# Performance work log

Hardware: AMD Instinct MI355X
Metric: run time of the kernel (lower is better)

## Reference

```python
import jax, jax.numpy as jnp
import numpy as np

N_EMBED = 1024
N_HEADS = 16


def setup_inputs() -> dict:
    key = jax.random.key(0)
    k_x, k_wa, k_wp = jax.random.split(key, 3)
    B, T, C = 2, 2048, N_EMBED
    x = jax.random.normal(k_x, (B, T, C), dtype=jnp.float32)
    # flax Dense default: lecun_normal kernel, zero bias; use scaled normal here
    w_attn = jax.random.normal(k_wa, (C, 3 * C), dtype=jnp.float32) / np.sqrt(C)
    b_attn = jnp.zeros((3 * C,), dtype=jnp.float32)
    w_proj = jax.random.normal(k_wp, (C, C), dtype=jnp.float32) / np.sqrt(C)
    b_proj = jnp.zeros((C,), dtype=jnp.float32)
    return {"x": x, "w_attn": w_attn, "b_attn": b_attn,
            "w_proj": w_proj, "b_proj": b_proj}


def reference(x, w_attn, b_attn, w_proj, b_proj):
    B, T, C = x.shape
    H = N_HEADS
    D = C // H
    qkv = x @ w_attn + b_attn                      # [B,T,3C]
    q, k, v = jnp.split(qkv, 3, axis=-1)           # each [B,T,C]
    q = q.reshape(B, T, H, D).swapaxes(1, 2)       # [B,H,T,D]
    k = k.reshape(B, T, H, D).swapaxes(1, 2)
    v = v.reshape(B, T, H, D).swapaxes(1, 2)
    att = jnp.einsum('bhid,bhjd->bhij', q, k) * (1.0 / jnp.sqrt(D))
    causal = jnp.tril(jnp.ones((T, T), dtype=bool))
    att = jnp.where(causal, att, -jnp.inf)
    att = jax.nn.softmax(att, axis=-1)
    y = jnp.einsum('bhij,bhjd->bhid', att, v)      # [B,H,T,D]
    y = y.swapaxes(1, 2).reshape(B, T, C)
    return y @ w_proj + b_proj
```

## Files before the change

### kernel.cpp

```cpp
#include <hip/hip_runtime.h>
#include <hip/hip_bf16.h>

typedef __bf16 bf16x8 __attribute__((ext_vector_type(8)));
typedef float f32x4 __attribute__((ext_vector_type(4)));
typedef float f32x16 __attribute__((ext_vector_type(16)));
typedef unsigned short u16;
typedef unsigned int u32;
typedef u16 u16x8 __attribute__((ext_vector_type(8)));
typedef u32 u32x4 __attribute__((ext_vector_type(4)));

#define SM_SCALE 0.1803368801111244f

__device__ inline u16 tobf(float f) {
  u32 u = __builtin_bit_cast(u32, f);
  u32 r = (u + 0x7fffu + ((u >> 16) & 1u)) >> 16;
  return (u16)r;
}

__device__ inline float frombf(u16 h) {
  return __builtin_bit_cast(float, (u32)h << 16);
}

__device__ inline void gload_lds16(const void* g, void* lds) {
  __builtin_amdgcn_global_load_lds(
      (const __attribute__((address_space(1))) u32*)g,
      (__attribute__((address_space(3))) u32*)lds, 16, 0, 0);
}

__global__ void convert_f32_bf16(const float* __restrict__ in,
                                 u16* __restrict__ out, int n8) {
  int i = blockIdx.x * blockDim.x + threadIdx.x;
  int stride = gridDim.x * blockDim.x;
  for (; i < n8; i += stride) {
    const float4* p = (const float4*)in + (size_t)i * 2;
    float4 a = p[0], b = p[1];
    u16x8 v;
    v[0] = tobf(a.x); v[1] = tobf(a.y); v[2] = tobf(a.z); v[3] = tobf(a.w);
    v[4] = tobf(b.x); v[5] = tobf(b.y); v[6] = tobf(b.z); v[7] = tobf(b.w);
    *(u16x8*)(out + (size_t)i * 8) = v;
  }
}

__global__ void transpose_w(const float* __restrict__ in,
                            u16* __restrict__ out, int K, int N) {
  __shared__ float tile[32][33];
  int nbx = N >> 5;
  int bx = blockIdx.x % nbx, by = blockIdx.x / nbx;
  int k0 = by << 5, n0 = bx << 5;
  int tx = threadIdx.x & 31, ty = threadIdx.x >> 5;
#pragma unroll
  for (int j = 0; j < 4; ++j) {
    int row = ty + j * 8;
    tile[row][tx] = in[(size_t)(k0 + row) * N + n0 + tx];
  }
  __syncthreads();
#pragma unroll
  for (int j = 0; j < 4; ++j) {
    int row = ty + j * 8;
    out[(size_t)(n0 + row) * K + k0 + tx] = tobf(tile[tx][row]);
  }
}

template <int EPI, int BN>
__global__ __launch_bounds__(256) void gemm_bt(
    const u16* __restrict__ A, const u16* __restrict__ Bt,
    const float* __restrict__ bias,
    u16* __restrict__ o0, u16* __restrict__ o1, u16* __restrict__ o2,
    float* __restrict__ fo, int M, int N, int K) {
  constexpr int NF = BN / 32;
  __shared__ __align__(16) u16 As[2][128 * 64];
  __shared__ __align__(16) u16 Bs[2][BN * 64];
  const int tid = threadIdx.x;
  const int lane = tid & 63;
  const int wave = tid >> 6;
  const int nbn = N / BN;
  int bid = (int)blockIdx.x;
  const int cpx = (int)gridDim.x >> 3;
  bid = (bid & 7) * cpx + (bid >> 3);
  const int bm = bid / nbn, bn = bid % nbn;
  const int m0 = bm << 7, n0 = bn * BN;
  const int wr = wave >> 1, wc = wave & 1;
  const int r15 = lane & 15, g = lane >> 4;

  f32x4 acc[4][NF] = {};

#define GSTAGE(buf, kt)                                                    \
  do {                                                                     \
    _Pragma("unroll")                                                      \
    for (int j = 0; j < 4; ++j) {                                          \
      int c = j * 4 + wave;                                                \
      int byte0 = c * 1024 + lane * 16;                                    \
      int row = byte0 >> 7;                                                \
      int colb = (byte0 & 127) ^ ((row & 7) << 4);                         \
      gload_lds16(A + (size_t)(m0 + row) * K + (kt) * 64 + (colb >> 1),    \
                  (char*)As[(buf)] + c * 1024);                            \
    }                                                                      \
    _Pragma("unroll")                                                      \
    for (int j = 0; j < NF; ++j) {                                         \
      int c = j * 4 + wave;                                                \
      int byte0 = c * 1024 + lane * 16;                                    \
      int row = byte0 >> 7;                                                \
      int colb = (byte0 & 127) ^ ((row & 7) << 4);                         \
      gload_lds16(Bt + (size_t)(n0 + row) * K + (kt) * 64 + (colb >> 1),   \
                  (char*)Bs[(buf)] + c * 1024);                            \
    }                                                                      \
  } while (0)

  const int nkt = K >> 6;
  GSTAGE(0, 0);
  asm volatile("s_waitcnt vmcnt(0)");
  __syncthreads();
  for (int kt = 0; kt < nkt; ++kt) {
    const int cur = kt & 1;
    if (kt + 1 < nkt) GSTAGE(cur ^ 1, kt + 1);
#pragma unroll
    for (int kk = 0; kk < 2; ++kk) {
      bf16x8 af[4], bf[NF];
#pragma unroll
      for (int i = 0; i < 4; ++i) {
        int rowA = wr * 64 + i * 16 + r15;
        int ca = (kk * 64 + 16 * g) ^ ((rowA & 7) << 4);
        af[i] = *(const bf16x8*)((const char*)As[cur] + rowA * 128 + ca);
      }
#pragma unroll
      for (int j2 = 0; j2 < NF; ++j2) {
        int rowB = wc * (BN / 2) + j2 * 16 + r15;
        int cb = (kk * 64 + 16 * g) ^ ((rowB & 7) << 4);
        bf[j2] = *(const bf16x8*)((const char*)Bs[cur] + rowB * 128 + cb);
      }
#pragma unroll
      for (int i = 0; i < 4; ++i)
#pragma unroll
        for (int j2 = 0; j2 < NF; ++j2)
          acc[i][j2] = __builtin_amdgcn_mfma_f32_16x16x32_bf16(
              af[i], bf[j2], acc[i][j2], 0, 0, 0);
    }
    asm volatile("s_waitcnt vmcnt(0)");
    __syncthreads();
  }
#undef GSTAGE

#pragma unroll
  for (int j2 = 0; j2 < NF; ++j2) {
    const int n = n0 + wc * (BN / 2) + j2 * 16 + r15;
    const float bv = bias[n];
#pragma unroll
    for (int i = 0; i < 4; ++i) {
      const int mb = m0 + wr * 64 + i * 16 + g * 4;
      float v[4];
#pragma unroll
      for (int rr = 0; rr < 4; ++rr) v[rr] = acc[i][j2][rr] + bv;
      if (EPI == 1) {
#pragma unroll
        for (int rr = 0; rr < 4; ++rr) fo[(size_t)(mb + rr) * N + n] = v[rr];
      } else {
        const int b = mb >> 11, t = mb & 2047;
        const int sec = n >> 10, nn = n & 1023;
        const int h = nn >> 6, d = nn & 63;
        const int bh = b * 16 + h;
        if (sec == 0) {
          u16* base = o0 + ((size_t)bh * 2048 + t) * 64 + d;
#pragma unroll
          for (int rr = 0; rr < 4; ++rr) base[rr * 64] = tobf(v[rr] * SM_SCALE);
        } else if (sec == 1) {
          u16* kb = o1 +
                    (((size_t)(bh * 32 + (t >> 6)) * 4 + (d >> 4)) * 2) * 512 +
                    ((d >> 3) & 1) * 256 + (d & 7);
          const int tb = t & 63;
#pragma unroll
          for (int rr = 0; rr < 4; ++rr) {
            int r = tb + rr;
            kb[(r >> 5) * 512 + (r & 31) * 8] = tobf(v[rr]);
          }
        } else {
          const int tl = t & 63;
          u16* vb = o2 +
                    ((((size_t)(bh * 32 + (t >> 6)) * 4 + (tl >> 4)) * 2 +
                      (d >> 5)) * 512) +
                    ((tl >> 3) & 1) * 256 + (d & 31) * 8 + (tl & 7);
          u32* p = (u32*)vb;
          p[0] = (u32)tobf(v[0]) | ((u32)tobf(v[1]) << 16);
          p[1] = (u32)tobf(v[2]) | ((u32)tobf(v[3]) << 16);
        }
      }
    }
  }
}

static __device__ const signed char PT_C[34] =
    {15,15,15,15,14,14,14,13,13,13,12,12,12,11,11,11,10,10,10,9,9,8,8,7,7,6,6,5,5,4,3,2,1,0};
static __device__ const signed char PT_K0[34] =
    {0,8,16,24,0,10,20,0,9,18,0,8,17,0,8,16,0,7,14,0,10,0,9,0,8,0,7,0,6,0,0,0,0,0};
static __device__ const signed char PT_KN[34] =
    {8,16,24,32,10,20,30,9,18,28,8,17,26,8,16,24,7,14,22,10,20,9,18,8,16,7,14,6,12,10,8,6,4,2};
static __device__ const signed char PT_SL[34] =
    {-1,0,1,2,-1,3,4,-1,5,6,-1,7,8,-1,9,10,-1,11,12,-1,13,-1,14,-1,15,-1,16,-1,17,-2,-2,-2,-2,-2};

__global__ __launch_bounds__(256) void attn_kernel(
    const u16* __restrict__ qb, const u16* __restrict__ kpk,
    const u16* __restrict__ vpk, u16* __restrict__ yb,
    u16* __restrict__ party, float* __restrict__ partM) {
  const int tid = threadIdx.x;
  const int lane = tid & 63;
  const int w = tid >> 6;
  const int q31 = lane & 31, hi = lane >> 5;
  const int bx = blockIdx.x;
  const int pid = bx >> 5, bh = bx & 31;
  const int c = PT_C[pid];
  const int kt0 = PT_K0[pid], ktN = PT_KN[pid];
  const int slot = PT_SL[pid];

  const int q0 = c * 128 + w * 32;
  const int qg = q0 + q31;
  const int qmax = q0 + 31;
  const int ktEnd = min(ktN, (qmax >> 6) + 1);

  const u16* qrow = qb + ((size_t)bh * 2048 + qg) * 64;
  bf16x8 aq[4];
#pragma unroll
  for (int ks = 0; ks < 4; ++ks)
    aq[ks] = *(const bf16x8*)(qrow + ks * 16 + 8 * hi);

  f32x16 o0 = {}, o1 = {};
  float m = -INFINITY, l = 0.f;

  const u16* kbh = kpk + (size_t)bh * 32 * 4096 + lane * 8;
  const u16* vbh = vpk + (size_t)bh * 32 * 4096 + lane * 8;

  for (int kt = kt0; kt < ktEnd; ++kt) {
    const u16* kp = kbh + (size_t)kt * 4096;
    const u16* vp = vbh + (size_t)kt * 4096;

    bf16x8 kf[8];
#pragma unroll
    for (int j = 0; j < 8; ++j) kf[j] = *(const bf16x8*)(kp + j * 512);

    f32x16 s0 = {}, s1 = {};
    __builtin_amdgcn_s_setprio(1);
#pragma unroll
    for (int ks = 0; ks < 4; ++ks) {
      s0 = __builtin_amdgcn_mfma_f32_32x32x16_bf16(kf[2 * ks], aq[ks], s0, 0, 0, 0);
      s1 = __builtin_amdgcn_mfma_f32_32x32x16_bf16(kf[2 * ks + 1], aq[ks], s1, 0, 0, 0);
    }
    __builtin_amdgcn_s_setprio(0);

    if (kt * 64 + 63 > q0) {
      const int thr = qg - kt * 64;
#pragma unroll
      for (int r = 0; r < 16; ++r) {
        const int off = (r & 3) + 8 * (r >> 2) + 4 * hi;
        if (off > thr) s0[r] = -INFINITY;
        if (off + 32 > thr) s1[r] = -INFINITY;
      }
    }
    f32x16 mx;
#pragma unroll
    for (int r = 0; r < 16; ++r) mx[r] = fmaxf(s0[r], s1[r]);
#pragma unroll
    for (int st = 8; st >= 1; st >>= 1)
#pragma unroll
      for (int r = 0; r < st; ++r) mx[r] = fmaxf(mx[r], mx[r + st]);
    float mt = fmaxf(mx[0], __shfl_xor(mx[0], 32, 64));

    if (kt == kt0) {
      m = mt;
    } else if (__any(mt > m + 8.f)) {
      float mnew = fmaxf(m, mt);
      float alpha = exp2f(m - mnew);
      m = mnew;
      l *= alpha;
#pragma unroll
      for (int r = 0; r < 16; ++r) {
        o0[r] *= alpha;
        o1[r] *= alpha;
      }
    }
#pragma unroll
    for (int r = 0; r < 16; ++r) {
      s0[r] = exp2f(s0[r] - m);
      s1[r] = exp2f(s1[r] - m);
    }
    {
      float la = 0.f, lb = 0.f, lc2 = 0.f, ld = 0.f;
#pragma unroll
      for (int r = 0; r < 16; r += 2) {
        la += s0[r];
        lb += s0[r + 1];
        lc2 += s1[r];
        ld += s1[r + 1];
      }
      l += (la + lb) + (lc2 + ld);
    }
    u32 W[16];
#pragma unroll
    for (int i2 = 0; i2 < 8; ++i2) {
      asm("v_cvt_pk_bf16_f32 %0, %1, %2"
          : "=v"(W[i2]) : "v"(s0[2 * i2]), "v"(s0[2 * i2 + 1]));
      asm("v_cvt_pk_bf16_f32 %0, %1, %2"
          : "=v"(W[8 + i2]) : "v"(s1[2 * i2]), "v"(s1[2 * i2 + 1]));
    }
#pragma unroll
    for (int b4 = 0; b4 < 16; b4 += 4) {
      asm("v_permlane32_swap_b32 %0, %1" : "+v"(W[b4]), "+v"(W[b4 + 2]));
      asm("v_permlane32_swap_b32 %0, %1" : "+v"(W[b4 + 1]), "+v"(W[b4 + 3]));
    }
    bf16x8 vf[8];
#pragma unroll
    for (int j = 0; j < 8; ++j) vf[j] = *(const bf16x8*)(vp + j * 512);

    __builtin_amdgcn_s_setprio(1);
#pragma unroll
    for (int ks = 0; ks < 4; ++ks) {
      u32x4 pwv = {W[4 * ks], W[4 * ks + 1], W[4 * ks + 2], W[4 * ks + 3]};
      bf16x8 pf = __builtin_bit_cast(bf16x8, pwv);
      o0 = __builtin_amdgcn_mfma_f32_32x32x16_bf16(vf[2 * ks], pf, o0, 0, 0, 0);
      o1 = __builtin_amdgcn_mfma_f32_32x32x16_bf16(vf[2 * ks + 1], pf, o1, 0, 0, 0);
    }
    __builtin_amdgcn_s_setprio(0);
  }

  l += __shfl_xor(l, 32, 64);
  float inv = 1.0f / l;

  u32* dst;
  if (slot >= 0) {
    dst = (u32*)(party +
                 ((size_t)((slot * 32 + bh) * 128 + w * 32 + q31)) * 64);
  } else {
    int b = bh >> 4, hd = bh & 15;
    dst = (u32*)(yb + ((size_t)b * 2048 + qg) * 1024 + hd * 64);
  }
#pragma unroll
  for (int r = 0; r < 16; r += 2) {
    int d = (r & 3) + 8 * (r >> 2) + 4 * hi;
    dst[d >> 1] = (u32)tobf(o0[r] * inv) | ((u32)tobf(o0[r + 1] * inv) << 16);
    dst[(d + 32) >> 1] =
        (u32)tobf(o1[r] * inv) | ((u32)tobf(o1[r + 1] * inv) << 16);
  }
  if (slot != -2 && hi == 0)
    partM[(pid * 32 + bh) * 128 + w * 32 + q31] = m + log2f(l);
}

static __device__ const signed char CB_PID[11] = {0,4,7,10,13,16,19,21,23,25,27};
static __device__ const signed char CB_P[11]   = {4,3,3,3,3,3,2,2,2,2,2};
static __device__ const signed char CB_SL[11]  = {0,3,5,7,9,11,13,14,15,16,17};

__global__ __launch_bounds__(256) void attn_combine(
    const u16* __restrict__ party, const float* __restrict__ partM,
    u16* __restrict__ yb) {
  const int gi = blockIdx.x;
  const int ci = gi >> 5, bh = gi & 31;
  const int c = 15 - ci;
  const int pidb = CB_PID[ci], P = CB_P[ci], slb = CB_SL[ci];
  const int row = threadIdx.x >> 1, off = (threadIdx.x & 1) * 32;

  const float M0 = partM[((pidb + 0) * 32 + bh) * 128 + row];
  const float M1 = partM[((pidb + 1) * 32 + bh) * 128 + row];
  const float M2 = (P > 2) ? partM[((pidb + 2) * 32 + bh) * 128 + row] : -INFINITY;
  const float M3 = (P > 3) ? partM[((pidb + 3) * 32 + bh) * 128 + row] : -INFINITY;
  const float Mm = fmaxf(fmaxf(M0, M1), fmaxf(M2, M3));
  const float w0 = exp2f(M0 - Mm), w1 = exp2f(M1 - Mm);
  const float w2 = exp2f(M2 - Mm), w3 = exp2f(M3 - Mm);
  const float inv = 1.f / (w0 + w1 + w2 + w3);

  const int b = bh >> 4, head = bh & 15, t = c * 128 + row;
  u16* y = yb + ((size_t)b * 2048 + t) * 1024 + head * 64 + off;

  float acc[32];
#pragma unroll
  for (int j = 0; j < 4; ++j) {
    u16x8 a = *(const u16x8*)(y + j * 8);
#pragma unroll
    for (int e = 0; e < 8; ++e) acc[j * 8 + e] = frombf(a[e]) * w0;
  }
  {
    const u16* p1 = party + ((size_t)((slb + 0) * 32 + bh) * 128 + row) * 64 + off;
#pragma unroll
    for (int j = 0; j < 4; ++j) {
      u16x8 a = *(const u16x8*)(p1 + j * 8);
#pragma unroll
      for (int e = 0; e < 8; ++e) acc[j * 8 + e] += frombf(a[e]) * w1;
    }
  }
  if (P > 2) {
    const u16* p2 = party + ((size_t)((slb + 1) * 32 + bh) * 128 + row) * 64 + off;
#pragma unroll
    for (int j = 0; j < 4; ++j) {
      u16x8 a = *(const u16x8*)(p2 + j * 8);
#pragma unroll
      for (int e = 0; e < 8; ++e) acc[j * 8 + e] += frombf(a[e]) * w2;
    }
  }
  if (P > 3) {
    const u16* p3 = party + ((size_t)((slb + 2) * 32 + bh) * 128 + row) * 64 + off;
#pragma unroll
    for (int j = 0; j < 4; ++j) {
      u16x8 a = *(const u16x8*)(p3 + j * 8);
#pragma unroll
      for (int e = 0; e < 8; ++e) acc[j * 8 + e] += frombf(a[e]) * w3;
    }
  }
#pragma unroll
  for (int j = 0; j < 4; ++j) {
    u16x8 ov;
#pragma unroll
    for (int e = 0; e < 8; ++e) ov[e] = tobf(acc[j * 8 + e] * inv);
    *(u16x8*)(y + j * 8) = ov;
  }
}

extern "C" void kernel_launch(void* const* d_in, const int* in_sizes, int n_in,
                              void* d_out, int out_size, void* d_ws,
                              size_t ws_size, hipStream_t stream) {
  const float* x = (const float*)d_in[0];
  const float* w_attn = (const float*)d_in[1];
  const float* b_attn = (const float*)d_in[2];
  const float* w_proj = (const float*)d_in[3];
  const float* b_proj = (const float*)d_in[4];
  float* out = (float*)d_out;
  char* ws = (char*)d_ws;

  u16* xb = (u16*)ws;
  u16* wat = (u16*)(ws + (8ull << 20));
  u16* wpt = (u16*)(ws + (14ull << 20));
  u16* qbuf = (u16*)(ws + (16ull << 20));
  u16* kpk = (u16*)(ws + (24ull << 20));
  u16* vpk = (u16*)(ws + (32ull << 20));
  u16* yb = (u16*)(ws + (40ull << 20));
  u16* party = (u16*)ws;
  float* partM = (float*)(ws + (10ull << 20));

  convert_f32_bf16<<<2048, 256, 0, stream>>>(x, xb, (4096 * 1024) / 8);
  transpose_w<<<3072, 256, 0, stream>>>(w_attn, wat, 1024, 3072);
  transpose_w<<<1024, 256, 0, stream>>>(w_proj, wpt, 1024, 1024);
  gemm_bt<0, 192><<<32 * 16, 256, 0, stream>>>(xb, wat, b_attn, qbuf, kpk,
                                               vpk, nullptr, 4096, 3072, 1024);
  attn_kernel<<<34 * 32, 256, 0, stream>>>(qbuf, kpk, vpk, yb, party, partM);
  attn_combine<<<352, 256, 0, stream>>>(party, partM, yb);
  gemm_bt<1, 64><<<32 * 16, 256, 0, stream>>>(yb, wpt, b_proj, nullptr,
                                              nullptr, nullptr, out, 4096,
                                              1024, 1024);
}
```

Measured before the change: 118.1 us.

## Merge prep kernels into one launch and double-buffer K loads in attention

Combines the x-to-bf16 conversion and the two weight transposes into a single prep kernel, removing two kernel launches and their gaps. In the attention loop, the next tile's K fragments are now prefetched into an alternating register buffer, and the V loads are issued right after the QK MFMAs, so global-load latency overlaps the softmax work. This raises register pressure through the extra K buffer, which could lower occupancy or cause spills.

```diff
diff --git a/kernel.cpp b/kernel.cpp
--- a/kernel.cpp
+++ b/kernel.cpp
@@ -27,27 +27,14 @@
       (__attribute__((address_space(3))) u32*)lds, 16, 0, 0);
 }
 
-__global__ void convert_f32_bf16(const float* __restrict__ in,
-                                 u16* __restrict__ out, int n8) {
-  int i = blockIdx.x * blockDim.x + threadIdx.x;
-  int stride = gridDim.x * blockDim.x;
-  for (; i < n8; i += stride) {
-    const float4* p = (const float4*)in + (size_t)i * 2;
-    float4 a = p[0], b = p[1];
-    u16x8 v;
-    v[0] = tobf(a.x); v[1] = tobf(a.y); v[2] = tobf(a.z); v[3] = tobf(a.w);
-    v[4] = tobf(b.x); v[5] = tobf(b.y); v[6] = tobf(b.z); v[7] = tobf(b.w);
-    *(u16x8*)(out + (size_t)i * 8) = v;
-  }
-}
-
-__global__ void transpose_w(const float* __restrict__ in,
-                            u16* __restrict__ out, int K, int N) {
+__device__ __forceinline__ void transpose_body(const float* __restrict__ in,
+                                               u16* __restrict__ out, int K,
+                                               int N, int bxg, int tid) {
   __shared__ float tile[32][33];
   int nbx = N >> 5;
-  int bx = blockIdx.x % nbx, by = blockIdx.x / nbx;
+  int bx = bxg % nbx, by = bxg / nbx;
   int k0 = by << 5, n0 = bx << 5;
-  int tx = threadIdx.x & 31, ty = threadIdx.x >> 5;
+  int tx = tid & 31, ty = tid >> 5;
 #pragma unroll
   for (int j = 0; j < 4; ++j) {
     int row = ty + j * 8;
@@ -58,6 +45,26 @@
   for (int j = 0; j < 4; ++j) {
     int row = ty + j * 8;
     out[(size_t)(n0 + row) * K + k0 + tx] = tobf(tile[tx][row]);
+  }
+}
+
+__global__ __launch_bounds__(256) void prep_kernel(
+    const float* __restrict__ x, u16* __restrict__ xb,
+    const float* __restrict__ wa, u16* __restrict__ wat,
+    const float* __restrict__ wp, u16* __restrict__ wpt) {
+  const int b = blockIdx.x, tid = threadIdx.x;
+  if (b < 2048) {
+    int i = b * 256 + tid;
+    const float4* p = (const float4*)x + (size_t)i * 2;
+    float4 a = p[0], c = p[1];
+    u16x8 v;
+    v[0] = tobf(a.x); v[1] = tobf(a.y); v[2] = tobf(a.z); v[3] = tobf(a.w);
+    v[4] = tobf(c.x); v[5] = tobf(c.y); v[6] = tobf(c.z); v[7] = tobf(c.w);
+    *(u16x8*)(xb + (size_t)i * 8) = v;
+  } else if (b < 5120) {
+    transpose_body(wa, wat, 1024, 3072, b - 2048, tid);
+  } else {
+    transpose_body(wp, wpt, 1024, 1024, b - 5120, tid);
   }
 }
 
@@ -196,6 +203,100 @@
 static __device__ const signed char PT_SL[34] =
     {-1,0,1,2,-1,3,4,-1,5,6,-1,7,8,-1,9,10,-1,11,12,-1,13,-1,14,-1,15,-1,16,-1,17,-2,-2,-2,-2,-2};
 
+__device__ __forceinline__ void attn_tile(
+    int kt, int kt0, int ktEnd, int q0, int qg, int hi,
+    const u16* __restrict__ kbh, const u16* __restrict__ vbh,
+    const bf16x8 (&aq)[4], const bf16x8 (&KF)[8], bf16x8 (&KN)[8],
+    bf16x8 (&vf)[8], f32x16& o0, f32x16& o1, float& m, float& l) {
+  f32x16 s0 = {}, s1 = {};
+  __builtin_amdgcn_s_setprio(1);
+#pragma unroll
+  for (int ks = 0; ks < 4; ++ks) {
+    s0 = __builtin_amdgcn_mfma_f32_32x32x16_bf16(KF[2 * ks], aq[ks], s0, 0, 0, 0);
+    s1 = __builtin_amdgcn_mfma_f32_32x32x16_bf16(KF[2 * ks + 1], aq[ks], s1, 0, 0, 0);
+  }
+  __builtin_amdgcn_s_setprio(0);
+
+  const u16* vp = vbh + (size_t)kt * 4096;
+#pragma unroll
+  for (int j = 0; j < 8; ++j) vf[j] = *(const bf16x8*)(vp + j * 512);
+  if (kt + 1 < ktEnd) {
+    const u16* kp2 = kbh + (size_t)(kt + 1) * 4096;
+#pragma unroll
+    for (int j = 0; j < 8; ++j) KN[j] = *(const bf16x8*)(kp2 + j * 512);
+  }
+
+  if (kt * 64 + 63 > q0) {
+    const int thr = qg - kt * 64;
+#pragma unroll
+    for (int r = 0; r < 16; ++r) {
+      const int off = (r & 3) + 8 * (r >> 2) + 4 * hi;
+      if (off > thr) s0[r] = -INFINITY;
+      if (off + 32 > thr) s1[r] = -INFINITY;
+    }
+  }
+  f32x16 mx;
+#pragma unroll
+  for (int r = 0; r < 16; ++r) mx[r] = fmaxf(s0[r], s1[r]);
+#pragma unroll
+  for (int st = 8; st >= 1; st >>= 1)
+#pragma unroll
+    for (int r = 0; r < st; ++r) mx[r] = fmaxf(mx[r], mx[r + st]);
+  float mt = fmaxf(mx[0], __shfl_xor(mx[0], 32, 64));
+
+  if (kt == kt0) {
+    m = mt;
+  } else if (__any(mt > m + 8.f)) {
+    float mnew = fmaxf(m, mt);
+    float alpha = exp2f(m - mnew);
+    m = mnew;
+    l *= alpha;
+#pragma unroll
+    for (int r = 0; r < 16; ++r) {
+      o0[r] *= alpha;
+      o1[r] *= alpha;
+    }
+  }
+#pragma unroll
+  for (int r = 0; r < 16; ++r) {
+    s0[r] = exp2f(s0[r] - m);
+    s1[r] = exp2f(s1[r] - m);
+  }
+  {
+    float la = 0.f, lb = 0.f, lc2 = 0.f, ld = 0.f;
+#pragma unroll
+    for (int r = 0; r < 16; r += 2) {
+      la += s0[r];
+      lb += s0[r + 1];
+      lc2 += s1[r];
+      ld += s1[r + 1];
+    }
+    l += (la + lb) + (lc2 + ld);
+  }
+  u32 W[16];
+#pragma unroll
+  for (int i2 = 0; i2 < 8; ++i2) {
+    asm("v_cvt_pk_bf16_f32 %0, %1, %2"
+        : "=v"(W[i2]) : "v"(s0[2 * i2]), "v"(s0[2 * i2 + 1]));
+    asm("v_cvt_pk_bf16_f32 %0, %1, %2"
+        : "=v"(W[8 + i2]) : "v"(s1[2 * i2]), "v"(s1[2 * i2 + 1]));
+  }
+#pragma unroll
+  for (int b4 = 0; b4 < 16; b4 += 4) {
+    asm("v_permlane32_swap_b32 %0, %1" : "+v"(W[b4]), "+v"(W[b4 + 2]));
+    asm("v_permlane32_swap_b32 %0, %1" : "+v"(W[b4 + 1]), "+v"(W[b4 + 3]));
+  }
+  __builtin_amdgcn_s_setprio(1);
+#pragma unroll
+  for (int ks = 0; ks < 4; ++ks) {
+    u32x4 pwv = {W[4 * ks], W[4 * ks + 1], W[4 * ks + 2], W[4 * ks + 3]};
+    bf16x8 pf = __builtin_bit_cast(bf16x8, pwv);
+    o0 = __builtin_amdgcn_mfma_f32_32x32x16_bf16(vf[2 * ks], pf, o0, 0, 0, 0);
+    o1 = __builtin_amdgcn_mfma_f32_32x32x16_bf16(vf[2 * ks + 1], pf, o1, 0, 0, 0);
+  }
+  __builtin_amdgcn_s_setprio(0);
+}
+
 __global__ __launch_bounds__(256) void attn_kernel(
     const u16* __restrict__ qb, const u16* __restrict__ kpk,
     const u16* __restrict__ vpk, u16* __restrict__ yb,
@@ -227,96 +328,19 @@
   const u16* kbh = kpk + (size_t)bh * 32 * 4096 + lane * 8;
   const u16* vbh = vpk + (size_t)bh * 32 * 4096 + lane * 8;
 
-  for (int kt = kt0; kt < ktEnd; ++kt) {
-    const u16* kp = kbh + (size_t)kt * 4096;
-    const u16* vp = vbh + (size_t)kt * 4096;
-
-    bf16x8 kf[8];
-#pragma unroll
-    for (int j = 0; j < 8; ++j) kf[j] = *(const bf16x8*)(kp + j * 512);
-
-    f32x16 s0 = {}, s1 = {};
-    __builtin_amdgcn_s_setprio(1);
-#pragma unroll
-    for (int ks = 0; ks < 4; ++ks) {
-      s0 = __builtin_amdgcn_mfma_f32_32x32x16_bf16(kf[2 * ks], aq[ks], s0, 0, 0, 0);
-      s1 = __builtin_amdgcn_mfma_f32_32x32x16_bf16(kf[2 * ks + 1], aq[ks], s1, 0, 0, 0);
-    }
-    __builtin_amdgcn_s_setprio(0);
-
-    if (kt * 64 + 63 > q0) {
-      const int thr = qg - kt * 64;
-#pragma unroll
-      for (int r = 0; r < 16; ++r) {
-        const int off = (r & 3) + 8 * (r >> 2) + 4 * hi;
-        if (off > thr) s0[r] = -INFINITY;
-        if (off + 32 > thr) s1[r] = -INFINITY;
-      }
-    }
-    f32x16 mx;
-#pragma unroll
-    for (int r = 0; r < 16; ++r) mx[r] = fmaxf(s0[r], s1[r]);
-#pragma unroll
-    for (int st = 8; st >= 1; st >>= 1)
-#pragma unroll
-      for (int r = 0; r < st; ++r) mx[r] = fmaxf(mx[r], mx[r + st]);
-    float mt = fmaxf(mx[0], __shfl_xor(mx[0], 32, 64));
-
-    if (kt == kt0) {
-      m = mt;
-    } else if (__any(mt > m + 8.f)) {
-      float mnew = fmaxf(m, mt);
-      float alpha = exp2f(m - mnew);
-      m = mnew;
-      l *= alpha;
-#pragma unroll
-      for (int r = 0; r < 16; ++r) {
-        o0[r] *= alpha;
-        o1[r] *= alpha;
-      }
-    }
-#pragma unroll
-    for (int r = 0; r < 16; ++r) {
-      s0[r] = exp2f(s0[r] - m);
-      s1[r] = exp2f(s1[r] - m);
-    }
-    {
-      float la = 0.f, lb = 0.f, lc2 = 0.f, ld = 0.f;
-#pragma unroll
-      for (int r = 0; r < 16; r += 2) {
-        la += s0[r];
-        lb += s0[r + 1];
-        lc2 += s1[r];
-        ld += s1[r + 1];
-      }
-      l += (la + lb) + (lc2 + ld);
-    }
-    u32 W[16];
-#pragma unroll
-    for (int i2 = 0; i2 < 8; ++i2) {
-      asm("v_cvt_pk_bf16_f32 %0, %1, %2"
-          : "=v"(W[i2]) : "v"(s0[2 * i2]), "v"(s0[2 * i2 + 1]));
-      asm("v_cvt_pk_bf16_f32 %0, %1, %2"
-          : "=v"(W[8 + i2]) : "v"(s1[2 * i2]), "v"(s1[2 * i2 + 1]));
-    }
-#pragma unroll
-    for (int b4 = 0; b4 < 16; b4 += 4) {
-      asm("v_permlane32_swap_b32 %0, %1" : "+v"(W[b4]), "+v"(W[b4 + 2]));
-      asm("v_permlane32_swap_b32 %0, %1" : "+v"(W[b4 + 1]), "+v"(W[b4 + 3]));
-    }
-    bf16x8 vf[8];
-#pragma unroll
-    for (int j = 0; j < 8; ++j) vf[j] = *(const bf16x8*)(vp + j * 512);
-
-    __builtin_amdgcn_s_setprio(1);
-#pragma unroll
-    for (int ks = 0; ks < 4; ++ks) {
-      u32x4 pwv = {W[4 * ks], W[4 * ks + 1], W[4 * ks + 2], W[4 * ks + 3]};
-      bf16x8 pf = __builtin_bit_cast(bf16x8, pwv);
-      o0 = __builtin_amdgcn_mfma_f32_32x32x16_bf16(vf[2 * ks], pf, o0, 0, 0, 0);
-      o1 = __builtin_amdgcn_mfma_f32_32x32x16_bf16(vf[2 * ks + 1], pf, o1, 0, 0, 0);
-    }
-    __builtin_amdgcn_s_setprio(0);
+  bf16x8 kfA[8], kfB[8], vf[8];
+  {
+    const u16* kp = kbh + (size_t)kt0 * 4096;
+#pragma unroll
+    for (int j = 0; j < 8; ++j) kfA[j] = *(const bf16x8*)(kp + j * 512);
+  }
+  int kt = kt0;
+  while (kt < ktEnd) {
+    attn_tile(kt, kt0, ktEnd, q0, qg, hi, kbh, vbh, aq, kfA, kfB, vf, o0, o1, m, l);
+    ++kt;
+    if (kt >= ktEnd) break;
+    attn_tile(kt, kt0, ktEnd, q0, qg, hi, kbh, vbh, aq, kfB, kfA, vf, o0, o1, m, l);
+    ++kt;
   }
 
   l += __shfl_xor(l, 32, 64);
@@ -430,9 +454,7 @@
   u16* party = (u16*)ws;
   float* partM = (float*)(ws + (10ull << 20));
 
-  convert_f32_bf16<<<2048, 256, 0, stream>>>(x, xb, (4096 * 1024) / 8);
-  transpose_w<<<3072, 256, 0, stream>>>(w_attn, wat, 1024, 3072);
-  transpose_w<<<1024, 256, 0, stream>>>(w_proj, wpt, 1024, 1024);
+  prep_kernel<<<6144, 256, 0, stream>>>(x, xb, w_attn, wat, w_proj, wpt);
   gemm_bt<0, 192><<<32 * 16, 256, 0, stream>>>(xb, wat, b_attn, qbuf, kpk,
                                                vpk, nullptr, 4096, 3072, 1024);
   attn_kernel<<<34 * 32, 256, 0, stream>>>(qbuf, kpk, vpk, yb, party, partM);
```

Measured after the change: 125.2 us. 6.0% more time.
